# Performance work log

Hardware: AMD Instinct MI355X
Metric: run time of the kernel (lower is better)

## Reference

```python
import jax, jax.numpy as jnp
import numpy as np

EMB = 1024
HEADS = 16
HEAD_SIZE = EMB // HEADS


def setup_inputs() -> dict:
    key = jax.random.key(0)
    ks = jax.random.split(key, 10)
    B, L = 2, 2048
    s = 1.0 / np.sqrt(EMB)
    inp = {
        "x": jax.random.normal(ks[0], (B, L, EMB), jnp.float32),
        "ln_g": jnp.ones((EMB,), jnp.float32),
        "ln_b": jnp.zeros((EMB,), jnp.float32),
        "Wq": jax.random.normal(ks[1], (EMB, EMB), jnp.float32) * s,
        "bq": jnp.zeros((EMB,), jnp.float32),
        "Wk": jax.random.normal(ks[2], (EMB, EMB), jnp.float32) * s,
        "bk": jnp.zeros((EMB,), jnp.float32),
        "Wv": jax.random.normal(ks[3], (EMB, EMB), jnp.float32) * s,
        "bv": jnp.zeros((EMB,), jnp.float32),
        "Wo": jax.random.normal(ks[4], (EMB, EMB), jnp.float32) * s,
        "bo": jnp.zeros((EMB,), jnp.float32),
    }
    return inp


def _attn_block(x, ln_g, ln_b, Wq, bq, Wk, bk, Wv, bv, Wo, bo):
    B, L, D = x.shape
    # LayerNorm (eps=1e-5 as torch default)
    mu = jnp.mean(x, axis=-1, keepdims=True)
    var = jnp.mean(jnp.square(x - mu), axis=-1, keepdims=True)
    h = (x - mu) * jax.lax.rsqrt(var + 1e-5) * ln_g + ln_b
    # QKV projections (torch Linear: x @ W.T + b), split heads -> [B,H,L,hs]
    def heads(y):
        return y.reshape(B, L, HEADS, HEAD_SIZE).transpose(0, 2, 1, 3)
    q = heads(h @ Wq.T + bq)
    k = heads(h @ Wk.T + bk)
    v = heads(h @ Wv.T + bv)
    # scaled dot-product attention (no mask; dropout = identity in eval)
    scores = jnp.einsum("bhqd,bhkd->bhqk", q, k) * (HEAD_SIZE ** -0.5)
    w = jax.nn.softmax(scores, axis=-1)
    o = jnp.einsum("bhqk,bhkd->bhqd", w, v)
    o = o.transpose(0, 2, 1, 3).reshape(B, L, D)
    return o @ Wo.T + bo


def reference(x, ln_g, ln_b, Wq, bq, Wk, bk, Wv, bv, Wo, bo):
    return _attn_block(x, ln_g, ln_b, Wq, bq, Wk, bk, Wv, bv, Wo, bo)
```

## Files before the change

### kernel.cpp

```cpp
#include <hip/hip_runtime.h>
#include <stdint.h>

#define EMB 1024
#define SEQL 2048
#define HEADS 16
#define HS 64

typedef __attribute__((ext_vector_type(8))) short bfx8;
typedef __attribute__((ext_vector_type(4))) float f32x4;
typedef __attribute__((ext_vector_type(16))) float f32x16;
typedef __attribute__((ext_vector_type(4))) unsigned short us4;
typedef __attribute__((ext_vector_type(8))) unsigned short us8;

__device__ __forceinline__ unsigned short f2bf(float f) {
  union { float f; unsigned u; } x; x.f = f;
  unsigned r = x.u + 0x7fffu + ((x.u >> 16) & 1u);
  return (unsigned short)(r >> 16);
}

__device__ __forceinline__ unsigned cvtpk(float lo, float hi) {
  unsigned r;
  asm("v_cvt_pk_bf16_f32 %0, %1, %2" : "=v"(r) : "v"(lo), "v"(hi));
  return r;
}

__device__ __forceinline__ float expv(float x) {
  float r;
  asm("v_exp_f32 %0, %1" : "=v"(r) : "v"(x));
  return r;
}

__device__ __forceinline__ float max3f(float a, float b, float c) {
  float r;
  asm("v_max3_f32 %0, %1, %2, %3" : "=v"(r) : "v"(a), "v"(b), "v"(c));
  return r;
}

__device__ __forceinline__ void gll16(const void* g, void* l) {
  __builtin_amdgcn_global_load_lds(
      (const __attribute__((address_space(1))) unsigned int*)g,
      (__attribute__((address_space(3))) unsigned int*)l, 16, 0, 0);
}

__global__ __launch_bounds__(256) void lncvt_kernel(
    const float* __restrict__ x, const float* __restrict__ gam,
    const float* __restrict__ bet, unsigned short* __restrict__ h,
    const float* __restrict__ s0, const float* __restrict__ s1,
    const float* __restrict__ s2, const float* __restrict__ s3,
    unsigned short* __restrict__ d) {
  const int tid = threadIdx.x;
  if (blockIdx.x < 4096) {
    const int row = blockIdx.x;
    const float4 v = reinterpret_cast<const float4*>(x + (size_t)row * EMB)[tid];
    float s = v.x + v.y + v.z + v.w;
    float sq = v.x * v.x + v.y * v.y + v.z * v.z + v.w * v.w;
    #pragma unroll
    for (int m = 1; m < 64; m <<= 1) {
      s += __shfl_xor(s, m, 64);
      sq += __shfl_xor(sq, m, 64);
    }
    __shared__ float red[8];
    const int lane = tid & 63, wave = tid >> 6;
    if (lane == 0) { red[wave] = s; red[wave + 4] = sq; }
    __syncthreads();
    s = red[0] + red[1] + red[2] + red[3];
    sq = red[4] + red[5] + red[6] + red[7];
    const float mu = s * (1.0f / EMB);
    const float var = sq * (1.0f / EMB) - mu * mu;
    const float rs = rsqrtf(var + 1e-5f);
    const float4 gg = reinterpret_cast<const float4*>(gam)[tid];
    const float4 bb = reinterpret_cast<const float4*>(bet)[tid];
    us4 o;
    o.x = f2bf((v.x - mu) * rs * gg.x + bb.x);
    o.y = f2bf((v.y - mu) * rs * gg.y + bb.y);
    o.z = f2bf((v.z - mu) * rs * gg.z + bb.z);
    o.w = f2bf((v.w - mu) * rs * gg.w + bb.w);
    reinterpret_cast<us4*>(h + (size_t)row * EMB)[tid] = o;
  } else {
    const int bid = blockIdx.x - 4096;
    const int m = bid >> 10;
    const int blk = bid & 1023;
    const float* s = (m == 0) ? s0 : (m == 1) ? s1 : (m == 2) ? s2 : s3;
    unsigned short* dd = d + (size_t)m * EMB * EMB;
    const int idx = blk * 256 + tid;
    const float4 v = reinterpret_cast<const float4*>(s)[idx];
    us4 o;
    o.x = f2bf(v.x); o.y = f2bf(v.y); o.z = f2bf(v.z); o.w = f2bf(v.w);
    reinterpret_cast<us4*>(dd)[idx] = o;
  }
}

__device__ __forceinline__ void gemm_tile(
    const unsigned short* __restrict__ Ag, const unsigned short* __restrict__ Bg,
    int m0, int n0, int K, char* lA, char* lB, f32x4 acc[4][4]) {
  const int tid = threadIdx.x;
  const int lane = tid & 63, wave = tid >> 6;
  const int g = lane >> 4, c = lane & 15;
  const int wr = wave >> 1, wc = wave & 1;

  const f32x4 zero = {0.f, 0.f, 0.f, 0.f};
  #pragma unroll
  for (int i = 0; i < 4; ++i)
    #pragma unroll
    for (int j = 0; j < 4; ++j) acc[i][j] = zero;

  const int Dbase = (wave * 4 * 64 + lane) * 16;
  for (int k0 = 0; k0 < K; k0 += 64) {
    __syncthreads();
    #pragma unroll
    for (int i = 0; i < 4; ++i) {
      const int Db = Dbase + i * 1024;
      const int row = Db >> 7;
      const int col = ((Db & 127) ^ ((row & 7) << 4)) >> 1;
      gll16(Ag + (size_t)(m0 + row) * K + (k0 + col), lA + (wave * 4 + i) * 1024);
      gll16(Bg + (size_t)(n0 + row) * K + (k0 + col), lB + (wave * 4 + i) * 1024);
    }
    __syncthreads();
    #pragma unroll
    for (int kf = 0; kf < 2; ++kf) {
      bfx8 af[4], bfr[4];
      #pragma unroll
      for (int i = 0; i < 4; ++i) {
        const int ra = wr * 64 + i * 16 + c;
        af[i] = *(const bfx8*)(lA + ra * 128 + ((kf * 64 + g * 16) ^ ((ra & 7) << 4)));
        const int rb = wc * 64 + i * 16 + c;
        bfr[i] = *(const bfx8*)(lB + rb * 128 + ((kf * 64 + g * 16) ^ ((rb & 7) << 4)));
      }
      #pragma unroll
      for (int i = 0; i < 4; ++i)
        #pragma unroll
        for (int j = 0; j < 4; ++j)
          acc[i][j] = __builtin_amdgcn_mfma_f32_16x16x32_bf16(af[i], bfr[j], acc[i][j], 0, 0, 0);
    }
  }
}

__device__ __forceinline__ void gemm_tile_n64(
    const unsigned short* __restrict__ Ag, const unsigned short* __restrict__ Bg,
    int m0, int n0, int K, char* lA, char* lB, f32x4 acc[4][2]) {
  const int tid = threadIdx.x;
  const int lane = tid & 63, wave = tid >> 6;
  const int g = lane >> 4, c = lane & 15;
  const int wr = wave >> 1, wc = wave & 1;

  const f32x4 zero = {0.f, 0.f, 0.f, 0.f};
  #pragma unroll
  for (int i = 0; i < 4; ++i)
    #pragma unroll
    for (int j = 0; j < 2; ++j) acc[i][j] = zero;

  const int DbaseA = (wave * 4 * 64 + lane) * 16;
  const int DbaseB = (wave * 2 * 64 + lane) * 16;
  for (int k0 = 0; k0 < K; k0 += 64) {
    __syncthreads();
    #pragma unroll
    for (int i = 0; i < 4; ++i) {
      const int Db = DbaseA + i * 1024;
      const int row = Db >> 7;
      const int col = ((Db & 127) ^ ((row & 7) << 4)) >> 1;
      gll16(Ag + (size_t)(m0 + row) * K + (k0 + col), lA + (wave * 4 + i) * 1024);
    }
    #pragma unroll
    for (int i = 0; i < 2; ++i) {
      const int Db = DbaseB + i * 1024;
      const int row = Db >> 7;
      const int col = ((Db & 127) ^ ((row & 7) << 4)) >> 1;
      gll16(Bg + (size_t)(n0 + row) * K + (k0 + col), lB + (wave * 2 + i) * 1024);
    }
    __syncthreads();
    #pragma unroll
    for (int kf = 0; kf < 2; ++kf) {
      bfx8 af[4], bfr[2];
      #pragma unroll
      for (int i = 0; i < 4; ++i) {
        const int ra = wr * 64 + i * 16 + c;
        af[i] = *(const bfx8*)(lA + ra * 128 + ((kf * 64 + g * 16) ^ ((ra & 7) << 4)));
      }
      #pragma unroll
      for (int j = 0; j < 2; ++j) {
        const int rb = wc * 32 + j * 16 + c;
        bfr[j] = *(const bfx8*)(lB + rb * 128 + ((kf * 64 + g * 16) ^ ((rb & 7) << 4)));
      }
      #pragma unroll
      for (int i = 0; i < 4; ++i)
        #pragma unroll
        for (int j = 0; j < 2; ++j)
          acc[i][j] = __builtin_amdgcn_mfma_f32_16x16x32_bf16(af[i], bfr[j], acc[i][j], 0, 0, 0);
    }
  }
}

__global__ __launch_bounds__(256, 3) void qkv_gemm(
    const unsigned short* __restrict__ h, const unsigned short* __restrict__ wbf,
    const float* __restrict__ bq, const float* __restrict__ bk,
    const float* __restrict__ bv, unsigned short* __restrict__ qb,
    unsigned short* __restrict__ kb, unsigned short* __restrict__ vtb) {
  __shared__ char lA[16384];
  __shared__ char lB[16384];
  f32x4 acc[4][4];
  const int m0 = blockIdx.x * 128;
  const int n0g = blockIdx.y * 128;
  const int mat = n0g >> 10;
  const int n0 = n0g & 1023;
  gemm_tile(h, wbf + (size_t)mat * EMB * EMB, m0, n0, EMB, lA, lB, acc);

  const float* bias = (mat == 0) ? bq : (mat == 1) ? bk : bv;
  const int tid = threadIdx.x;
  const int lane = tid & 63, wave = tid >> 6;
  const int g = lane >> 4, c = lane & 15;
  const int wr = wave >> 1, wc = wave & 1;

  if (mat < 2) {
    #pragma unroll
    for (int i = 0; i < 4; ++i) {
      #pragma unroll
      for (int j = 0; j < 4; ++j) {
        const int col = n0 + wc * 64 + j * 16 + c;
        const float bz = bias[col];
        const int hh = col >> 6, d = col & 63;
        #pragma unroll
        for (int r = 0; r < 4; ++r) {
          const int row = m0 + wr * 64 + i * 16 + 4 * g + r;
          const int bidx = row >> 11, l = row & 2047;
          const unsigned short bv16 = f2bf(acc[i][j][r] + bz);
          unsigned short* dst = (mat == 0) ? qb : kb;
          dst[(((size_t)(bidx * HEADS + hh) * SEQL + l) << 6) + d] = bv16;
        }
      }
    }
  } else {
    __syncthreads();
    char* wbase = (wc ? lB : lA);
    #pragma unroll
    for (int i = 0; i < 4; ++i) {
      #pragma unroll
      for (int j = 0; j < 4; ++j) {
        const int colL = wc * 64 + j * 16 + c;
        const float bz = bias[n0 + colL];
        uint2 w;
        w.x = cvtpk(acc[i][j][0] + bz, acc[i][j][1] + bz);
        w.y = cvtpk(acc[i][j][2] + bz, acc[i][j][3] + bz);
        const int off = (wr * 128 + i * 32 + 8 * g) ^ ((colL & 7) << 4);
        *reinterpret_cast<uint2*>(wbase + (colL & 63) * 256 + off) = w;
      }
    }
    __syncthreads();
    const char* rbase = (wave >= 2) ? lB : lA;
    const int colbase = ((wave >= 2) ? 64 : 0) + (wave & 1) * 32;
    const int g0 = lane & 15;
    const int bidx = m0 >> 11;
    const int l0 = (m0 & 2047) + g0 * 8;
    #pragma unroll
    for (int dc = 0; dc < 8; ++dc) {
      const int colL = colbase + dc * 4 + (lane >> 4);
      const int slot = g0 ^ (colL & 7);
      const us8 v = *reinterpret_cast<const us8*>(
          rbase + (colL & 63) * 256 + slot * 16);
      const int colG = n0 + colL;
      const int hh = colG >> 6, d = colG & 63;
      *reinterpret_cast<us8*>(
          vtb + ((size_t)(bidx * HEADS + hh) * HS + d) * SEQL + l0) = v;
    }
  }
}

__global__ __launch_bounds__(256, 2) void attn_kernel(
    const unsigned short* __restrict__ qb, const unsigned short* __restrict__ kb,
    const unsigned short* __restrict__ vtb, unsigned short* __restrict__ ob) {
  __shared__ char lK[4][8192];
  __shared__ char lV[4][8192];
  const int tid = threadIdx.x, lane = tid & 63, wave = tid >> 6;
  const int l31 = lane & 31, hi = lane >> 5;
  const int sw = (l31 & 7) << 4;
  const int qblk = blockIdx.x;
  const int bh = blockIdx.y;
  const unsigned short* qp = qb + (size_t)bh * SEQL * HS;
  const unsigned short* kp = kb + (size_t)bh * SEQL * HS;
  const unsigned short* vp = vtb + (size_t)bh * HS * SEQL;
  const int qbase = qblk * 128 + wave * 32;

  bfx8 aq[4];
  #pragma unroll
  for (int kf = 0; kf < 4; ++kf)
    aq[kf] = *(const bfx8*)(qp + (size_t)(qbase + l31) * HS + kf * 16 + hi * 8);

  const float SCL = 0.125f * 1.44269504089f;
  const float THR = 11.5416f;
  const bfx8 vone = {0x3F80, 0x3F80, 0x3F80, 0x3F80, 0x3F80, 0x3F80, 0x3F80, 0x3F80};

  float mst = 0.0f;
  f32x16 oacc0, oacc1, lacc;
  f32x16 spa, spb;
  const f32x16 zero16 = {0.f,0.f,0.f,0.f,0.f,0.f,0.f,0.f,0.f,0.f,0.f,0.f,0.f,0.f,0.f,0.f};
  oacc0 = zero16; oacc1 = zero16; lacc = zero16;
  spa = zero16; spb = zero16;

  const int sbase = wave * 2048;
  const int Db0 = sbase + lane * 16, Db1 = Db0 + 1024;
  const int sr0 = Db0 >> 7, sr1 = Db1 >> 7;
  const int sc0 = ((Db0 & 127) ^ ((sr0 & 7) << 4)) >> 1;
  const int sc1 = ((Db1 & 127) ^ ((sr1 & 7) << 4)) >> 1;
  const unsigned short* k0s = kp + (size_t)sr0 * HS + sc0;
  const unsigned short* k1s = kp + (size_t)sr1 * HS + sc1;
  const unsigned short* v0s = vp + (size_t)sr0 * SEQL + sc0;
  const unsigned short* v1s = vp + (size_t)sr1 * SEQL + sc1;

  gll16(k0s, lK[0] + sbase); gll16(k1s, lK[0] + sbase + 1024);
  gll16(v0s, lV[0] + sbase); gll16(v1s, lV[0] + sbase + 1024);
  gll16(k0s + 64 * HS, lK[1] + sbase); gll16(k1s + 64 * HS, lK[1] + sbase + 1024);
  gll16(v0s + 64, lV[1] + sbase); gll16(v1s + 64, lV[1] + sbase + 1024);

  const unsigned short* kf0 = k0s + 2 * 64 * HS;
  const unsigned short* kf1 = k1s + 2 * 64 * HS;
  const unsigned short* vf0 = v0s + 2 * 64;
  const unsigned short* vf1 = v1s + 2 * 64;

  auto qk_half = [&](const char* kptr) -> f32x16 {
    f32x16 s;
    {
      const bfx8 a0 = *(const bfx8*)(kptr + l31 * 128 + ((16 * hi) ^ sw));
      s = __builtin_amdgcn_mfma_f32_32x32x16_bf16(a0, aq[0], zero16, 0, 0, 0);
    }
    #pragma unroll
    for (int kf = 1; kf < 4; ++kf) {
      const int ko = (32 * kf + 16 * hi) ^ sw;
      const bfx8 a0 = *(const bfx8*)(kptr + l31 * 128 + ko);
      s = __builtin_amdgcn_mfma_f32_32x32x16_bf16(a0, aq[kf], s, 0, 0, 0);
    }
    return s;
  };

  auto smpv = [&](f32x16& s, const char* lVc, const int kfv) {
    bfx8 vb0, vb1, vb2, vb3;
    {
      const int vo0 = (32 * kfv + 16 * hi) ^ sw;
      const int vo1 = (32 * (kfv + 1) + 16 * hi) ^ sw;
      vb0 = *(const bfx8*)(lVc + l31 * 128 + vo0);
      vb1 = *(const bfx8*)(lVc + l31 * 128 + 4096 + vo0);
      vb2 = *(const bfx8*)(lVc + l31 * 128 + vo1);
      vb3 = *(const bfx8*)(lVc + l31 * 128 + 4096 + vo1);
    }

    float m0 = max3f(s[0], s[1], s[2]);
    float m1 = max3f(s[3], s[4], s[5]);
    float m2 = max3f(s[6], s[7], s[8]);
    float m3 = max3f(s[9], s[10], s[11]);
    float m4 = max3f(s[12], s[13], s[14]);
    m0 = max3f(m0, m1, m2);
    m3 = max3f(m3, m4, s[15]);
    const float sm = fmaxf(m0, m3);

    if (__any(sm * SCL > mst + THR)) {
      float mt = sm * SCL;
      mt = fmaxf(mt, __shfl_xor(mt, 32, 64));
      const float mn = fmaxf(mst, mt);
      const float al = exp2f(mst - mn);
      mst = mn;
      #pragma unroll
      for (int r = 0; r < 16; ++r) {
        const int qi = (r & 3) + 8 * (r >> 2) + 4 * hi;
        const float alq = __shfl(al, qi, 64);
        lacc[r] *= alq;
        oacc0[r] *= alq;
        oacc1[r] *= alq;
      }
    }

    #pragma unroll
    for (int r = 0; r < 16; ++r) s[r] = expv(fmaf(s[r], SCL, -mst));

    __builtin_amdgcn_s_setprio(1);
    #pragma unroll
    for (int h2 = 0; h2 < 2; ++h2) {
      const int bb = 8 * h2;
      unsigned w0 = cvtpk(s[bb + 0], s[bb + 1]), w2 = cvtpk(s[bb + 4], s[bb + 5]);
      unsigned w1 = cvtpk(s[bb + 2], s[bb + 3]), w3 = cvtpk(s[bb + 6], s[bb + 7]);
      asm("v_permlane32_swap_b32 %0, %1" : "+v"(w0), "+v"(w2));
      asm("v_permlane32_swap_b32 %0, %1" : "+v"(w1), "+v"(w3));
      union { unsigned u[4]; bfx8 v; } pa;
      pa.u[0] = w0; pa.u[1] = w1; pa.u[2] = w2; pa.u[3] = w3;
      lacc = __builtin_amdgcn_mfma_f32_32x32x16_bf16(pa.v, vone, lacc, 0, 0, 0);
      const bfx8 b0 = h2 ? vb2 : vb0;
      const bfx8 b1 = h2 ? vb3 : vb1;
      oacc0 = __builtin_amdgcn_mfma_f32_32x32x16_bf16(pa.v, b0, oacc0, 0, 0, 0);
      oacc1 = __builtin_amdgcn_mfma_f32_32x32x16_bf16(pa.v, b1, oacc1, 0, 0, 0);
    }
    __builtin_amdgcn_s_setprio(0);
  };

  auto step = [&](const char* lKc, const char* lVp, char* nK, char* nV,
                  const int wait, const bool doStage, const bool doSMPV) {
    if (wait == 4) asm volatile("s_waitcnt vmcnt(4)" ::: "memory");
    else           asm volatile("s_waitcnt vmcnt(0)" ::: "memory");
    __builtin_amdgcn_s_barrier();
    __builtin_amdgcn_sched_barrier(0);
    if (doStage) {
      gll16(kf0, nK + sbase); gll16(kf1, nK + sbase + 1024);
      gll16(vf0, nV + sbase); gll16(vf1, nV + sbase + 1024);
      kf0 += 64 * HS; kf1 += 64 * HS; vf0 += 64; vf1 += 64;
    }
    __builtin_amdgcn_s_setprio(1);
    f32x16 na = qk_half(lKc);
    f32x16 nb = qk_half(lKc + 4096);
    __builtin_amdgcn_s_setprio(0);
    if (doSMPV) {
      smpv(spa, lVp, 0);
      smpv(spb, lVp, 2);
    }
    spa = na; spb = nb;
  };

  step(lK[0], lV[3], lK[2], lV[2], 4, true, false);
  for (int g4 = 0; g4 < 7; ++g4) {
    step(lK[1], lV[0], lK[3], lV[3], 4, true, true);
    step(lK[2], lV[1], lK[0], lV[0], 4, true, true);
    step(lK[3], lV[2], lK[1], lV[1], 4, true, true);
    step(lK[0], lV[3], lK[2], lV[2], 4, true, true);
  }
  step(lK[1], lV[0], lK[3], lV[3], 4, true, true);
  step(lK[2], lV[1], lK[0], lV[0], 4, false, true);
  step(lK[3], lV[2], lK[0], lV[0], 0, false, true);
  smpv(spa, lV[3], 0);
  smpv(spb, lV[3], 2);

  const int b = bh >> 4, hh = bh & 15;
  #pragma unroll
  for (int r = 0; r < 16; ++r) {
    const float inv = 1.f / lacc[r];
    const int row = qbase + (r & 3) + 8 * (r >> 2) + 4 * hi;
    unsigned short* orow = ob + (size_t)(b * SEQL + row) * EMB + hh * 64;
    orow[l31] = f2bf(oacc0[r] * inv);
    orow[32 + l31] = f2bf(oacc1[r] * inv);
  }
}

__global__ __launch_bounds__(256, 2) void out_gemm(
    const unsigned short* __restrict__ ob, const unsigned short* __restrict__ wo,
    const float* __restrict__ bo, float* __restrict__ out) {
  __shared__ char lA[16384];
  __shared__ char lB[8192];
  f32x4 acc[4][2];
  const int m0 = blockIdx.x * 128;
  const int n0 = blockIdx.y * 64;
  gemm_tile_n64(ob, wo, m0, n0, EMB, lA, lB, acc);

  const int lane = threadIdx.x & 63, wave = threadIdx.x >> 6;
  const int g = lane >> 4, c = lane & 15;
  const int wr = wave >> 1, wc = wave & 1;
  #pragma unroll
  for (int i = 0; i < 4; ++i)
    #pragma unroll
    for (int j = 0; j < 2; ++j) {
      const int col = n0 + wc * 32 + j * 16 + c;
      const float bz = bo[col];
      #pragma unroll
      for (int r = 0; r < 4; ++r) {
        const int row = m0 + wr * 64 + i * 16 + 4 * g + r;
        out[(size_t)row * EMB + col] = acc[i][j][r] + bz;
      }
    }
}

extern "C" void kernel_launch(void* const* d_in, const int* in_sizes, int n_in,
                              void* d_out, int out_size, void* d_ws, size_t ws_size,
                              hipStream_t stream) {
  const float* x   = (const float*)d_in[0];
  const float* lng = (const float*)d_in[1];
  const float* lnb = (const float*)d_in[2];
  const float* Wq  = (const float*)d_in[3];
  const float* bq  = (const float*)d_in[4];
  const float* Wk  = (const float*)d_in[5];
  const float* bk  = (const float*)d_in[6];
  const float* Wv  = (const float*)d_in[7];
  const float* bv  = (const float*)d_in[8];
  const float* Wo  = (const float*)d_in[9];
  const float* bo  = (const float*)d_in[10];

  char* ws = (char*)d_ws;
  unsigned short* h   = (unsigned short*)(ws);
  unsigned short* wbf = (unsigned short*)(ws + 8388608);
  unsigned short* qb  = (unsigned short*)(ws + 16777216);
  unsigned short* kb  = (unsigned short*)(ws + 25165824);
  unsigned short* vtb = (unsigned short*)(ws + 33554432);
  unsigned short* ob  = (unsigned short*)(ws + 41943040);
  float* out = (float*)d_out;

  lncvt_kernel<<<dim3(8192), dim3(256), 0, stream>>>(x, lng, lnb, h,
                                                     Wq, Wk, Wv, Wo, wbf);
  qkv_gemm<<<dim3(32, 24), dim3(256), 0, stream>>>(h, wbf, bq, bk, bv, qb, kb, vtb);
  attn_kernel<<<dim3(16, 32), dim3(256), 0, stream>>>(qb, kb, vtb, ob);
  out_gemm<<<dim3(32, 16), dim3(256), 0, stream>>>(ob, wbf + (size_t)3 * EMB * EMB, bo, out);
}
```

Baseline: 112.9 us.

## Pre-swizzle K and V^T in global memory with 8-byte XOR granularity

Moves the XOR swizzle out of the attention kernel's global-to-LDS copy and into the projection epilogue, which now writes K and V^T to global memory in a swizzled order at 8-byte granularity (XOR with the row index mod 16). The attention kernel then copies contiguously into LDS and reads each 16-byte MFMA operand as two 8-byte LDS loads. The aim is fewer LDS bank conflicts and simpler address arithmetic for the loads. The cost is twice as many LDS read instructions and a scattered element-wise store pattern in the K epilogue.

```diff
diff --git a/kernel.cpp b/kernel.cpp
--- a/kernel.cpp
+++ b/kernel.cpp
@@ -40,6 +40,13 @@
   __builtin_amdgcn_global_load_lds(
       (const __attribute__((address_space(1))) unsigned int*)g,
       (__attribute__((address_space(3))) unsigned int*)l, 16, 0, 0);
+}
+
+__device__ __forceinline__ bfx8 ld2(const char* rowbase, int j, int sx) {
+  union { uint2 u[2]; bfx8 v; } x;
+  x.u[0] = *(const uint2*)(rowbase + ((j ^ sx) << 3));
+  x.u[1] = *(const uint2*)(rowbase + (((j + 1) ^ sx) << 3));
+  return x.v;
 }
 
 __global__ __launch_bounds__(256) void lncvt_kernel(
@@ -223,8 +230,12 @@
           const int row = m0 + wr * 64 + i * 16 + 4 * g + r;
           const int bidx = row >> 11, l = row & 2047;
           const unsigned short bv16 = f2bf(acc[i][j][r] + bz);
-          unsigned short* dst = (mat == 0) ? qb : kb;
-          dst[(((size_t)(bidx * HEADS + hh) * SEQL + l) << 6) + d] = bv16;
+          if (mat == 0) {
+            qb[(((size_t)(bidx * HEADS + hh) * SEQL + l) << 6) + d] = bv16;
+          } else {
+            kb[(((size_t)(bidx * HEADS + hh) * SEQL + l) << 6) +
+               (((d >> 2) ^ (l & 15)) << 2) + (d & 3)] = bv16;
+          }
         }
       }
     }
@@ -258,8 +269,13 @@
           rbase + (colL & 63) * 256 + slot * 16);
       const int colG = n0 + colL;
       const int hh = colG >> 6, d = colG & 63;
-      *reinterpret_cast<us8*>(
-          vtb + ((size_t)(bidx * HEADS + hh) * HS + d) * SEQL + l0) = v;
+      const int sx = d & 15;
+      const int j0 = (l0 & 63) >> 2;
+      uint2* vrow = reinterpret_cast<uint2*>(
+          vtb + ((size_t)(bidx * HEADS + hh) * HS + d) * SEQL + (l0 & ~63));
+      union { us8 v8; uint2 u2[2]; } uu; uu.v8 = v;
+      vrow[j0 ^ sx] = uu.u2[0];
+      vrow[(j0 ^ sx) ^ 1] = uu.u2[1];
     }
   }
 }
@@ -271,7 +287,7 @@
   __shared__ char lV[4][8192];
   const int tid = threadIdx.x, lane = tid & 63, wave = tid >> 6;
   const int l31 = lane & 31, hi = lane >> 5;
-  const int sw = (l31 & 7) << 4;
+  const int sx = l31 & 15;
   const int qblk = blockIdx.x;
   const int bh = blockIdx.y;
   const unsigned short* qp = qb + (size_t)bh * SEQL * HS;
@@ -296,14 +312,11 @@
   spa = zero16; spb = zero16;
 
   const int sbase = wave * 2048;
-  const int Db0 = sbase + lane * 16, Db1 = Db0 + 1024;
-  const int sr0 = Db0 >> 7, sr1 = Db1 >> 7;
-  const int sc0 = ((Db0 & 127) ^ ((sr0 & 7) << 4)) >> 1;
-  const int sc1 = ((Db1 & 127) ^ ((sr1 & 7) << 4)) >> 1;
-  const unsigned short* k0s = kp + (size_t)sr0 * HS + sc0;
-  const unsigned short* k1s = kp + (size_t)sr1 * HS + sc1;
-  const unsigned short* v0s = vp + (size_t)sr0 * SEQL + sc0;
-  const unsigned short* v1s = vp + (size_t)sr1 * SEQL + sc1;
+  const int X0 = sbase + lane * 16, X1 = X0 + 1024;
+  const unsigned short* k0s = kp + (X0 >> 1);
+  const unsigned short* k1s = kp + (X1 >> 1);
+  const unsigned short* v0s = vp + (size_t)(X0 >> 7) * SEQL + ((X0 & 127) >> 1);
+  const unsigned short* v1s = vp + (size_t)(X1 >> 7) * SEQL + ((X1 & 127) >> 1);
 
   gll16(k0s, lK[0] + sbase); gll16(k1s, lK[0] + sbase + 1024);
   gll16(v0s, lV[0] + sbase); gll16(v1s, lV[0] + sbase + 1024);
@@ -317,29 +330,26 @@
 
   auto qk_half = [&](const char* kptr) -> f32x16 {
     f32x16 s;
+    const char* rb = kptr + l31 * 128;
     {
-      const bfx8 a0 = *(const bfx8*)(kptr + l31 * 128 + ((16 * hi) ^ sw));
+      const bfx8 a0 = ld2(rb, 2 * hi, sx);
       s = __builtin_amdgcn_mfma_f32_32x32x16_bf16(a0, aq[0], zero16, 0, 0, 0);
     }
     #pragma unroll
     for (int kf = 1; kf < 4; ++kf) {
-      const int ko = (32 * kf + 16 * hi) ^ sw;
-      const bfx8 a0 = *(const bfx8*)(kptr + l31 * 128 + ko);
+      const bfx8 a0 = ld2(rb, 4 * kf + 2 * hi, sx);
       s = __builtin_amdgcn_mfma_f32_32x32x16_bf16(a0, aq[kf], s, 0, 0, 0);
     }
     return s;
   };
 
   auto smpv = [&](f32x16& s, const char* lVc, const int kfv) {
-    bfx8 vb0, vb1, vb2, vb3;
-    {
-      const int vo0 = (32 * kfv + 16 * hi) ^ sw;
-      const int vo1 = (32 * (kfv + 1) + 16 * hi) ^ sw;
-      vb0 = *(const bfx8*)(lVc + l31 * 128 + vo0);
-      vb1 = *(const bfx8*)(lVc + l31 * 128 + 4096 + vo0);
-      vb2 = *(const bfx8*)(lVc + l31 * 128 + vo1);
-      vb3 = *(const bfx8*)(lVc + l31 * 128 + 4096 + vo1);
-    }
+    const char* rb0 = lVc + l31 * 128;
+    const char* rb1 = rb0 + 4096;
+    const bfx8 vb0 = ld2(rb0, 4 * kfv + 2 * hi, sx);
+    const bfx8 vb1 = ld2(rb1, 4 * kfv + 2 * hi, sx);
+    const bfx8 vb2 = ld2(rb0, 4 * (kfv + 1) + 2 * hi, sx);
+    const bfx8 vb3 = ld2(rb1, 4 * (kfv + 1) + 2 * hi, sx);
 
     float m0 = max3f(s[0], s[1], s[2]);
     float m1 = max3f(s[3], s[4], s[5]);
```

Result: slower. 117.4 us (+3.9%).
